# Kernel tuning notes

Measured on AMD Instinct MI355X. Metric: run time of the kernel, lower is better.

The kernel has to match this reference:

```python
import jax, jax.numpy as jnp
import numpy as np

H, B, T, DH = 16, 2, 2048, 64
MODEL_DIM = 1024


def setup_inputs() -> dict:
    key = jax.random.key(0)
    ks = jax.random.split(key, 5)
    q = jax.random.normal(ks[0], (H, B, T, DH), dtype=jnp.float32)
    k = jax.random.normal(ks[1], (H, B, T, DH), dtype=jnp.float32)
    v = jax.random.normal(ks[2], (H, B, T, DH), dtype=jnp.float32)
    Wo_w = jax.random.normal(ks[3], (MODEL_DIM, H * DH), dtype=jnp.float32) * 0.02
    Wo_b = jax.random.normal(ks[4], (MODEL_DIM,), dtype=jnp.float32) * 0.02
    return {"q": q, "k": k, "v": v, "Wo_w": Wo_w, "Wo_b": Wo_b}


def reference(q, k, v, Wo_w, Wo_b):
    # per-head scaled dot-product attention; scale uses per-head dk (=DH)
    scale = jnp.sqrt(jnp.asarray(DH, dtype=q.dtype))
    # scores: [H, B, T, T]
    scores = jnp.einsum('hbtd,hbsd->hbts', q, k) / scale
    # causal mask (additive -1e12 on strict upper triangle, matching torch code)
    mask = jnp.triu(jnp.ones((T, T), dtype=bool), 1)
    scores = scores + (-1e12) * mask.astype(scores.dtype)
    weights = jax.nn.softmax(scores, axis=-1)
    # context per head: [H, B, T, DH]
    context = jnp.einsum('hbts,hbsd->hbtd', weights, v)
    # concat heads along feature dim: [B, T, H*DH]
    context = jnp.transpose(context, (1, 2, 0, 3)).reshape(B, T, H * DH)
    # output projection (torch Linear: x @ W.T + b)
    return context @ Wo_w.T + Wo_b
```

## Files before the change

### kernel.cpp

```cpp
#include <hip/hip_runtime.h>

typedef __attribute__((ext_vector_type(8))) short bf16x8;
typedef __attribute__((ext_vector_type(4))) float f32x4;
typedef __attribute__((ext_vector_type(4))) unsigned int u32x4;
typedef __attribute__((ext_vector_type(2))) unsigned int u32x2;
typedef __attribute__((ext_vector_type(4))) unsigned short u16x4;

#define H_ 16
#define B_ 2
#define T_ 2048
#define DH_ 64
#define MD_ 1024

static __device__ inline unsigned short f2bf(float f) {
    union { float f; unsigned u; } x; x.f = f;
    unsigned r = (x.u + 0x7fffu + ((x.u >> 16) & 1u)) >> 16;
    return (unsigned short)r;
}
static __device__ inline unsigned int pack_bf2(float lo, float hi) {
    return __builtin_amdgcn_perm(__float_as_uint(hi), __float_as_uint(lo), 0x07060302u);
}
static __device__ inline float fexp2(float x) {
#if __has_builtin(__builtin_amdgcn_exp2f)
    return __builtin_amdgcn_exp2f(x);
#else
    return exp2f(x);
#endif
}

__global__ __launch_bounds__(256) void prep_k(const float* __restrict__ k,
                                              const float* __restrict__ v,
                                              const float* __restrict__ w,
                                              unsigned short* __restrict__ kb,
                                              unsigned short* __restrict__ vtb,
                                              unsigned short* __restrict__ wob,
                                              int* __restrict__ fl) {
    __shared__ __attribute__((aligned(16))) unsigned short vt64[64][64];
    const int blk = blockIdx.x;
    const int tid = threadIdx.x;
    if (blk < 1024) {
        int i = (blk * 256 + tid) * 4;
        f32x4 x = *(const f32x4*)(w + i);
        u16x4 y;
        y[0] = f2bf(x[0]); y[1] = f2bf(x[1]); y[2] = f2bf(x[2]); y[3] = f2bf(x[3]);
        *(u16x4*)(wob + i) = y;
    } else if (blk < 2048) {
        int j = blk - 1024;
        const int hb = j >> 5, s0 = (j & 31) * 64;
        const int row = tid >> 2, c = (tid & 3) * 16;
        const long off = (long)hb * (T_ * DH_) + (long)(s0 + row) * DH_ + c;
        const float* p = k + off;
        f32x4 a0 = *(const f32x4*)p;
        f32x4 a1 = *(const f32x4*)(p + 4);
        f32x4 a2 = *(const f32x4*)(p + 8);
        f32x4 a3 = *(const f32x4*)(p + 12);
        u32x4 w0, w1;
        w0[0] = pack_bf2(a0[0], a0[1]); w0[1] = pack_bf2(a0[2], a0[3]);
        w0[2] = pack_bf2(a1[0], a1[1]); w0[3] = pack_bf2(a1[2], a1[3]);
        w1[0] = pack_bf2(a2[0], a2[1]); w1[1] = pack_bf2(a2[2], a2[3]);
        w1[2] = pack_bf2(a3[0], a3[1]); w1[3] = pack_bf2(a3[2], a3[3]);
        *(u32x4*)(kb + off) = w0;
        *(u32x4*)(kb + off + 8) = w1;
    } else if (blk < 3072) {
        int j = blk - 2048;
        const int hb = j >> 5, s0 = (j & 31) * 64;
        const int vkp = tid & 31, vdg = tid >> 5;
        const float* vp = v + (long)hb * (T_ * DH_) + (long)(s0 + 2 * vkp) * DH_ + vdg * 8;
        f32x4 va0 = *(const f32x4*)vp;
        f32x4 va1 = *(const f32x4*)(vp + 4);
        f32x4 vb0 = *(const f32x4*)(vp + DH_);
        f32x4 vb1 = *(const f32x4*)(vp + DH_ + 4);
#pragma unroll
        for (int jj = 0; jj < 4; jj++) {
            ((unsigned int*)&vt64[vdg * 8 + jj][0])[vkp]     = pack_bf2(va0[jj], vb0[jj]);
            ((unsigned int*)&vt64[vdg * 8 + 4 + jj][0])[vkp] = pack_bf2(va1[jj], vb1[jj]);
        }
        __syncthreads();
        const int dh = tid >> 2, kc = (tid & 3) * 16;
        u32x4 o0 = *(const u32x4*)&vt64[dh][kc];
        u32x4 o1 = *(const u32x4*)&vt64[dh][kc + 8];
        unsigned short* op = vtb + (long)hb * (DH_ * T_) + (long)dh * T_ + s0 + kc;
        *(u32x4*)op = o0;
        *(u32x4*)(op + 8) = o1;
    } else {
        for (int z = tid; z < 512; z += 256) fl[z] = 0;
    }
}

#define SE(t, lo, hi) ((unsigned)((t) | ((lo) << 8) | ((hi) << 16)))
__constant__ unsigned sched48[48] = {
    SE(31,0,16), SE(31,16,32), SE(30,15,31), SE(15,0,16),
    SE(30,0,15), SE(29,0,15), SE(29,15,30), SE(28,14,29), SE(14,0,15),
    SE(28,0,14), SE(27,0,14), SE(27,14,28), SE(26,13,27), SE(13,0,14),
    SE(26,0,13), SE(25,0,13), SE(25,13,26), SE(24,12,25), SE(12,0,13),
    SE(24,0,12), SE(23,0,12), SE(23,12,24), SE(22,11,23), SE(11,0,12),
    SE(22,0,11), SE(21,0,11), SE(21,11,22), SE(20,10,21), SE(10,0,11),
    SE(20,0,10), SE(19,0,10), SE(19,10,20), SE(18,9,19), SE(9,0,10),
    SE(18,0,9), SE(17,0,9), SE(17,9,18), SE(16,8,17), SE(8,0,9),
    SE(16,0,8), SE(7,0,8),
    SE(6,0,7), SE(5,0,6), SE(4,0,5), SE(3,0,4), SE(2,0,3), SE(1,0,2), SE(0,0,1)
};

__global__ __launch_bounds__(256, 4) void attn_k(const float* __restrict__ q,
                                                 const unsigned short* __restrict__ kb,
                                                 const unsigned short* __restrict__ vtb,
                                                 unsigned short* __restrict__ ctx,
                                                 float* __restrict__ Op,
                                                 float* __restrict__ lp,
                                                 int* __restrict__ fl) {
    const int i = blockIdx.x;
    const int xcd = i & 7, j = i >> 3;
    const int l = j & 3, idx = j >> 2;
    const unsigned e = sched48[idx];
    const int t  = (int)(e & 255u);
    const int lo = (int)((e >> 8) & 255u);
    const int hi = (int)(e >> 16);
    const int hb = xcd * 4 + l;
    const int h = hb >> 1, b = hb & 1;
    const int tid = threadIdx.x;
    const int wave = tid >> 6, lane = tid & 63;
    const int ln = lane & 15, quad = lane >> 4;

    __shared__ __attribute__((aligned(16))) unsigned short kt[64][72];
    __shared__ __attribute__((aligned(16))) unsigned short vt[64][72];
    __shared__ __attribute__((aligned(16))) unsigned short pl[4][16][72];
    __shared__ int sh_who;

    const long kbase = (long)hb * (T_ * DH_);
    const long vbase = (long)hb * (DH_ * T_);
    const int q0w = t * 64 + wave * 16;
    const int srow = tid >> 2, sc = (tid & 3) * 16;

    bf16x8 qf0, qf1;
    {
        const float qs = 0.18033688011112042f;
        const float* qp = q + kbase + (long)(q0w + ln) * DH_ + quad * 8;
        f32x4 a0 = *(const f32x4*)qp;
        f32x4 a1 = *(const f32x4*)(qp + 4);
        f32x4 b0 = *(const f32x4*)(qp + 32);
        f32x4 b1 = *(const f32x4*)(qp + 36);
#pragma unroll
        for (int z = 0; z < 4; z++) {
            qf0[z]   = (short)f2bf(a0[z] * qs);
            qf0[4+z] = (short)f2bf(a1[z] * qs);
            qf1[z]   = (short)f2bf(b0[z] * qs);
            qf1[4+z] = (short)f2bf(b1[z] * qs);
        }
    }

    f32x4 oT[4];
#pragma unroll
    for (int z = 0; z < 4; z++) oT[z] = f32x4{0.f, 0.f, 0.f, 0.f};
    float lsum = 0.f;

    u32x4 kr0, kr1, vr0, vr1;
    {
        const unsigned short* kp = kb + kbase + (long)(lo * 64 + srow) * DH_ + sc;
        kr0 = *(const u32x4*)kp; kr1 = *(const u32x4*)(kp + 8);
        const unsigned short* vp = vtb + vbase + (long)srow * T_ + lo * 64 + sc;
        vr0 = *(const u32x4*)vp; vr1 = *(const u32x4*)(vp + 8);
    }

#pragma unroll 1
    for (int step = lo; step < hi; step++) {
        __syncthreads();
        *(u32x4*)&kt[srow][sc]     = kr0;
        *(u32x4*)&kt[srow][sc + 8] = kr1;
        *(u32x4*)&vt[srow][sc]     = vr0;
        *(u32x4*)&vt[srow][sc + 8] = vr1;
        __syncthreads();

        if (step + 1 < hi) {
            const unsigned short* kp = kb + kbase + (long)((step + 1) * 64 + srow) * DH_ + sc;
            kr0 = *(const u32x4*)kp; kr1 = *(const u32x4*)(kp + 8);
            const unsigned short* vp = vtb + vbase + (long)srow * T_ + (step + 1) * 64 + sc;
            vr0 = *(const u32x4*)vp; vr1 = *(const u32x4*)(vp + 8);
        }

        f32x4 sa[4];
#pragma unroll
        for (int nt = 0; nt < 4; nt++) {
            bf16x8 kf0 = *(const bf16x8*)&kt[nt * 16 + ln][quad * 8];
            bf16x8 kf1 = *(const bf16x8*)&kt[nt * 16 + ln][32 + quad * 8];
            f32x4 a = f32x4{0.f, 0.f, 0.f, 0.f};
            a = __builtin_amdgcn_mfma_f32_16x16x32_bf16(kf0, qf0, a, 0, 0, 0);
            a = __builtin_amdgcn_mfma_f32_16x16x32_bf16(kf1, qf1, a, 0, 0, 0);
            sa[nt] = a;
        }

        if (step == t) {
            const int qi = wave * 16 + ln;
#pragma unroll
            for (int nt = 0; nt < 4; nt++)
#pragma unroll
                for (int r = 0; r < 4; r++) {
                    float p = fexp2(sa[nt][r]);
                    if (nt * 16 + quad * 4 + r > qi) p = 0.f;
                    sa[nt][r] = p;
                }
        } else {
#pragma unroll
            for (int nt = 0; nt < 4; nt++)
#pragma unroll
                for (int r = 0; r < 4; r++)
                    sa[nt][r] = fexp2(sa[nt][r]);
        }

#pragma unroll
        for (int nt = 0; nt < 4; nt++)
            lsum += (sa[nt][0] + sa[nt][1]) + (sa[nt][2] + sa[nt][3]);

#pragma unroll
        for (int nt = 0; nt < 4; nt++) {
            u32x2 ww;
            ww[0] = pack_bf2(sa[nt][0], sa[nt][1]);
            ww[1] = pack_bf2(sa[nt][2], sa[nt][3]);
            *(u32x2*)&pl[wave][ln][nt * 16 + quad * 4] = ww;
        }

        bf16x8 pf0 = *(const bf16x8*)&pl[wave][ln][quad * 8];
        bf16x8 pf1 = *(const bf16x8*)&pl[wave][ln][32 + quad * 8];

#pragma unroll
        for (int dt = 0; dt < 4; dt++) {
            bf16x8 vf0 = *(const bf16x8*)&vt[dt * 16 + ln][quad * 8];
            bf16x8 vf1 = *(const bf16x8*)&vt[dt * 16 + ln][32 + quad * 8];
            oT[dt] = __builtin_amdgcn_mfma_f32_16x16x32_bf16(vf0, pf0, oT[dt], 0, 0, 0);
            oT[dt] = __builtin_amdgcn_mfma_f32_16x16x32_bf16(vf1, pf1, oT[dt], 0, 0, 0);
        }
    }

    lsum += __shfl_xor(lsum, 16);
    lsum += __shfl_xor(lsum, 32);

    float rl;
    if (t < 16) {
        rl = __builtin_amdgcn_rcpf(lsum);
    } else {
        const int c = (lo != 0) ? 1 : 0;
        const long slab = (((long)c * 32 + hb) * 16 + (t - 16));
        float* ob = Op + slab * 4096;
        const int qlocal = wave * 16 + ln;
#pragma unroll
        for (int dt = 0; dt < 4; dt++)
#pragma unroll
            for (int r = 0; r < 4; r++)
                __hip_atomic_store(&ob[(dt * 16 + quad * 4 + r) * 64 + qlocal], oT[dt][r],
                                   __ATOMIC_RELAXED, __HIP_MEMORY_SCOPE_AGENT);
        if (quad == 0)
            __hip_atomic_store(&lp[slab * 64 + qlocal], lsum,
                               __ATOMIC_RELAXED, __HIP_MEMORY_SCOPE_AGENT);
        __syncthreads();
        if (tid == 0)
            sh_who = __hip_atomic_fetch_add(&fl[hb * 16 + (t - 16)], 1,
                                            __ATOMIC_RELAXED, __HIP_MEMORY_SCOPE_AGENT);
        __syncthreads();
        if (sh_who != 1) return;
        const long slab2 = (((long)(c ^ 1) * 32 + hb) * 16 + (t - 16));
        const float* qb = Op + slab2 * 4096;
#pragma unroll
        for (int dt = 0; dt < 4; dt++)
#pragma unroll
            for (int r = 0; r < 4; r++)
                oT[dt][r] += __hip_atomic_load(&qb[(dt * 16 + quad * 4 + r) * 64 + qlocal],
                                               __ATOMIC_RELAXED, __HIP_MEMORY_SCOPE_AGENT);
        lsum += __hip_atomic_load(&lp[slab2 * 64 + qlocal],
                                  __ATOMIC_RELAXED, __HIP_MEMORY_SCOPE_AGENT);
        rl = __builtin_amdgcn_rcpf(lsum);
    }

#pragma unroll
    for (int dt = 0; dt < 4; dt++) {
        u16x4 y;
        y[0] = f2bf(oT[dt][0] * rl); y[1] = f2bf(oT[dt][1] * rl);
        y[2] = f2bf(oT[dt][2] * rl); y[3] = f2bf(oT[dt][3] * rl);
        *(u16x4*)&pl[wave][ln][dt * 16 + quad * 4] = y;
    }
    const int rr = lane >> 2, cc = (lane & 3) * 16;
    u32x4 z0 = *(const u32x4*)&pl[wave][rr][cc];
    u32x4 z1 = *(const u32x4*)&pl[wave][rr][cc + 8];
    unsigned short* cp = ctx + (long)(b * T_ + t * 64 + wave * 16 + rr) * MD_ + h * 64 + cc;
    *(u32x4*)cp = z0;
    *(u32x4*)(cp + 8) = z1;
}

__global__ __launch_bounds__(256, 4) void proj_k(const unsigned short* __restrict__ A,
                                                 const unsigned short* __restrict__ Bw,
                                                 const float* __restrict__ bias,
                                                 float* __restrict__ out) {
    const int i = blockIdx.x;
    const int n0 = ((i & 7) * 2 + ((i >> 3) & 1)) * 64;
    const int m0 = (i >> 4) * 64;
    const int tid = threadIdx.x;
    const int wave = tid >> 6, lane = tid & 63;
    const int ln = lane & 15, quad = lane >> 4;

    __shared__ __attribute__((aligned(16))) unsigned short As[64][72];
    __shared__ __attribute__((aligned(16))) unsigned short Bs[64][72];

    const int srow = tid >> 2, sc = (tid & 3) * 16;

    f32x4 acc[4];
#pragma unroll
    for (int z = 0; z < 4; z++) acc[z] = f32x4{0.f, 0.f, 0.f, 0.f};

    u32x4 ar0, ar1, br0, br1;
    {
        const unsigned short* ap = A + (long)(m0 + srow) * 1024 + sc;
        ar0 = *(const u32x4*)ap; ar1 = *(const u32x4*)(ap + 8);
        const unsigned short* bp = Bw + (long)(n0 + srow) * 1024 + sc;
        br0 = *(const u32x4*)bp; br1 = *(const u32x4*)(bp + 8);
    }

#pragma unroll 1
    for (int ks = 0; ks < 1024; ks += 64) {
        __syncthreads();
        *(u32x4*)&As[srow][sc]     = ar0;
        *(u32x4*)&As[srow][sc + 8] = ar1;
        *(u32x4*)&Bs[srow][sc]     = br0;
        *(u32x4*)&Bs[srow][sc + 8] = br1;
        __syncthreads();

        if (ks + 64 < 1024) {
            const unsigned short* ap = A + (long)(m0 + srow) * 1024 + ks + 64 + sc;
            ar0 = *(const u32x4*)ap; ar1 = *(const u32x4*)(ap + 8);
            const unsigned short* bp = Bw + (long)(n0 + srow) * 1024 + ks + 64 + sc;
            br0 = *(const u32x4*)bp; br1 = *(const u32x4*)(bp + 8);
        }

        bf16x8 bf0 = *(const bf16x8*)&Bs[wave * 16 + ln][quad * 8];
        bf16x8 bf1 = *(const bf16x8*)&Bs[wave * 16 + ln][32 + quad * 8];
#pragma unroll
        for (int mt = 0; mt < 4; mt++) {
            bf16x8 af0 = *(const bf16x8*)&As[mt * 16 + ln][quad * 8];
            bf16x8 af1 = *(const bf16x8*)&As[mt * 16 + ln][32 + quad * 8];
            acc[mt] = __builtin_amdgcn_mfma_f32_16x16x32_bf16(af0, bf0, acc[mt], 0, 0, 0);
            acc[mt] = __builtin_amdgcn_mfma_f32_16x16x32_bf16(af1, bf1, acc[mt], 0, 0, 0);
        }
    }

    int col = n0 + wave * 16 + ln;
    float bz = bias[col];
#pragma unroll
    for (int mt = 0; mt < 4; mt++)
#pragma unroll
        for (int r = 0; r < 4; r++) {
            int row = m0 + mt * 16 + quad * 4 + r;
            out[(long)row * 1024 + col] = acc[mt][r] + bz;
        }
}

extern "C" void kernel_launch(void* const* d_in, const int* in_sizes, int n_in,
                              void* d_out, int out_size, void* d_ws, size_t ws_size,
                              hipStream_t stream) {
    const float* q    = (const float*)d_in[0];
    const float* k    = (const float*)d_in[1];
    const float* v    = (const float*)d_in[2];
    const float* Wo_w = (const float*)d_in[3];
    const float* Wo_b = (const float*)d_in[4];
    float* out = (float*)d_out;

    unsigned short* ctx = (unsigned short*)d_ws;
    unsigned short* wob = ctx + (size_t)4096 * 1024;
    unsigned short* kbb = wob + (size_t)1024 * 1024;
    unsigned short* vtb = kbb + (size_t)32 * 2048 * 64;
    float* Opart = (float*)(vtb + (size_t)32 * 2048 * 64);
    float* lpart = Opart + (size_t)2 * 32 * 16 * 64 * 64;
    int*   flags = (int*)(lpart + (size_t)2 * 32 * 16 * 64);

    prep_k<<<3073, 256, 0, stream>>>(k, v, Wo_w, kbb, vtb, wob, flags);
    attn_k<<<1536, 256, 0, stream>>>(q, kbb, vtb, ctx, Opart, lpart, flags);
    proj_k<<<1024, 256, 0, stream>>>(ctx, wob, Wo_b, out);
}
```

Measured before the change: 150.8 us.

## Double attention query tile to 128 rows and rebalance causal work schedule

Each attention block now processes 128 query rows, with each wave handling two 16-row subtiles, so every K/V tile staged in shared memory feeds twice as many MFMAs. The static causal schedule is rebuilt as a 3-slot by 8-type table so work balances across CUs with 768 blocks, and long rows are still split in two with a combine through partial buffers. Occupancy drops to 3 blocks per CU, register pressure rises from the doubled accumulators, and fully masked K tiles are skipped per wave.

```diff
diff --git a/kernel.cpp b/kernel.cpp
--- a/kernel.cpp
+++ b/kernel.cpp
@@ -83,25 +83,21 @@
         *(u32x4*)op = o0;
         *(u32x4*)(op + 8) = o1;
     } else {
-        for (int z = tid; z < 512; z += 256) fl[z] = 0;
-    }
-}
-
-#define SE(t, lo, hi) ((unsigned)((t) | ((lo) << 8) | ((hi) << 16)))
-__constant__ unsigned sched48[48] = {
-    SE(31,0,16), SE(31,16,32), SE(30,15,31), SE(15,0,16),
-    SE(30,0,15), SE(29,0,15), SE(29,15,30), SE(28,14,29), SE(14,0,15),
-    SE(28,0,14), SE(27,0,14), SE(27,14,28), SE(26,13,27), SE(13,0,14),
-    SE(26,0,13), SE(25,0,13), SE(25,13,26), SE(24,12,25), SE(12,0,13),
-    SE(24,0,12), SE(23,0,12), SE(23,12,24), SE(22,11,23), SE(11,0,12),
-    SE(22,0,11), SE(21,0,11), SE(21,11,22), SE(20,10,21), SE(10,0,11),
-    SE(20,0,10), SE(19,0,10), SE(19,10,20), SE(18,9,19), SE(9,0,10),
-    SE(18,0,9), SE(17,0,9), SE(17,9,18), SE(16,8,17), SE(8,0,9),
-    SE(16,0,8), SE(7,0,8),
-    SE(6,0,7), SE(5,0,6), SE(4,0,5), SE(3,0,4), SE(2,0,3), SE(1,0,2), SE(0,0,1)
+        for (int z = tid; z < 256; z += 256) fl[z] = 0;
+    }
+}
+
+#define SE2(t, lo, hi) ((unsigned)((t) | ((lo) << 4) | ((hi) << 10)))
+__constant__ unsigned sched24[3][8] = {
+    { SE2(15,0,16), SE2(7,0,16), SE2(14,0,15), SE2(14,15,30),
+      SE2(13,0,14), SE2(13,14,28), SE2(12,13,26), SE2(11,12,24) },
+    { SE2(15,16,32), SE2(6,0,14), SE2(12,0,13), SE2(10,0,11),
+      SE2(10,11,22), SE2(9,0,10), SE2(11,0,12), SE2(5,0,12) },
+    { SE2(0,0,2), SE2(1,0,4), SE2(2,0,6), SE2(3,0,8),
+      SE2(8,0,9), SE2(9,10,20), SE2(8,9,18), SE2(4,0,10) },
 };
 
-__global__ __launch_bounds__(256, 4) void attn_k(const float* __restrict__ q,
+__global__ __launch_bounds__(256, 3) void attn_k(const float* __restrict__ q,
                                                  const unsigned short* __restrict__ kb,
                                                  const unsigned short* __restrict__ vtb,
                                                  unsigned short* __restrict__ ctx,
@@ -110,12 +106,13 @@
                                                  int* __restrict__ fl) {
     const int i = blockIdx.x;
     const int xcd = i & 7, j = i >> 3;
-    const int l = j & 3, idx = j >> 2;
-    const unsigned e = sched48[idx];
-    const int t  = (int)(e & 255u);
-    const int lo = (int)((e >> 8) & 255u);
-    const int hi = (int)(e >> 16);
-    const int hb = xcd * 4 + l;
+    const int cu = j & 31, slot = j >> 5;
+    const int type = cu >> 2, hbl = cu & 3;
+    const unsigned e = sched24[slot][type];
+    const int t  = (int)(e & 15u);
+    const int lo = (int)((e >> 4) & 63u);
+    const int hi = (int)(e >> 10);
+    const int hb = xcd * 4 + hbl;
     const int h = hb >> 1, b = hb & 1;
     const int tid = threadIdx.x;
     const int wave = tid >> 6, lane = tid & 63;
@@ -123,35 +120,44 @@
 
     __shared__ __attribute__((aligned(16))) unsigned short kt[64][72];
     __shared__ __attribute__((aligned(16))) unsigned short vt[64][72];
-    __shared__ __attribute__((aligned(16))) unsigned short pl[4][16][72];
+    __shared__ __attribute__((aligned(16))) unsigned short pl[4][32][72];
     __shared__ int sh_who;
 
     const long kbase = (long)hb * (T_ * DH_);
     const long vbase = (long)hb * (DH_ * T_);
-    const int q0w = t * 64 + wave * 16;
+    const int q0w = t * 128 + wave * 32;
     const int srow = tid >> 2, sc = (tid & 3) * 16;
 
-    bf16x8 qf0, qf1;
+    bf16x8 qf00, qf01, qf10, qf11;
     {
         const float qs = 0.18033688011112042f;
-        const float* qp = q + kbase + (long)(q0w + ln) * DH_ + quad * 8;
-        f32x4 a0 = *(const f32x4*)qp;
-        f32x4 a1 = *(const f32x4*)(qp + 4);
-        f32x4 b0 = *(const f32x4*)(qp + 32);
-        f32x4 b1 = *(const f32x4*)(qp + 36);
+        const float* qp0 = q + kbase + (long)(q0w + ln) * DH_ + quad * 8;
+        const float* qp1 = qp0 + 16 * DH_;
+        f32x4 a0 = *(const f32x4*)qp0;
+        f32x4 a1 = *(const f32x4*)(qp0 + 4);
+        f32x4 b0 = *(const f32x4*)(qp0 + 32);
+        f32x4 b1 = *(const f32x4*)(qp0 + 36);
+        f32x4 c0 = *(const f32x4*)qp1;
+        f32x4 c1 = *(const f32x4*)(qp1 + 4);
+        f32x4 d0 = *(const f32x4*)(qp1 + 32);
+        f32x4 d1 = *(const f32x4*)(qp1 + 36);
 #pragma unroll
         for (int z = 0; z < 4; z++) {
-            qf0[z]   = (short)f2bf(a0[z] * qs);
-            qf0[4+z] = (short)f2bf(a1[z] * qs);
-            qf1[z]   = (short)f2bf(b0[z] * qs);
-            qf1[4+z] = (short)f2bf(b1[z] * qs);
-        }
-    }
-
-    f32x4 oT[4];
-#pragma unroll
-    for (int z = 0; z < 4; z++) oT[z] = f32x4{0.f, 0.f, 0.f, 0.f};
-    float lsum = 0.f;
+            qf00[z]   = (short)f2bf(a0[z] * qs);
+            qf00[4+z] = (short)f2bf(a1[z] * qs);
+            qf01[z]   = (short)f2bf(b0[z] * qs);
+            qf01[4+z] = (short)f2bf(b1[z] * qs);
+            qf10[z]   = (short)f2bf(c0[z] * qs);
+            qf10[4+z] = (short)f2bf(c1[z] * qs);
+            qf11[z]   = (short)f2bf(d0[z] * qs);
+            qf11[4+z] = (short)f2bf(d1[z] * qs);
+        }
+    }
+
+    f32x4 oT0[4], oT1[4];
+#pragma unroll
+    for (int z = 0; z < 4; z++) { oT0[z] = f32x4{0.f,0.f,0.f,0.f}; oT1[z] = f32x4{0.f,0.f,0.f,0.f}; }
+    float lsum0 = 0.f, lsum1 = 0.f;
 
     u32x4 kr0, kr1, vr0, vr1;
     {
@@ -177,111 +183,129 @@
             vr0 = *(const u32x4*)vp; vr1 = *(const u32x4*)(vp + 8);
         }
 
-        f32x4 sa[4];
-#pragma unroll
-        for (int nt = 0; nt < 4; nt++) {
-            bf16x8 kf0 = *(const bf16x8*)&kt[nt * 16 + ln][quad * 8];
-            bf16x8 kf1 = *(const bf16x8*)&kt[nt * 16 + ln][32 + quad * 8];
-            f32x4 a = f32x4{0.f, 0.f, 0.f, 0.f};
-            a = __builtin_amdgcn_mfma_f32_16x16x32_bf16(kf0, qf0, a, 0, 0, 0);
-            a = __builtin_amdgcn_mfma_f32_16x16x32_bf16(kf1, qf1, a, 0, 0, 0);
-            sa[nt] = a;
-        }
-
-        if (step == t) {
-            const int qi = wave * 16 + ln;
-#pragma unroll
-            for (int nt = 0; nt < 4; nt++)
-#pragma unroll
-                for (int r = 0; r < 4; r++) {
-                    float p = fexp2(sa[nt][r]);
-                    if (nt * 16 + quad * 4 + r > qi) p = 0.f;
-                    sa[nt][r] = p;
+        if (step * 64 <= q0w + 31) {
+            const bool dmask = (step * 64 + 63 > q0w);
+            const int dbase = step * 64 + quad * 4 - q0w - ln;
+
+#pragma unroll
+            for (int nt = 0; nt < 4; nt++) {
+                bf16x8 kf0 = *(const bf16x8*)&kt[nt * 16 + ln][quad * 8];
+                bf16x8 kf1 = *(const bf16x8*)&kt[nt * 16 + ln][32 + quad * 8];
+                f32x4 a0 = f32x4{0.f,0.f,0.f,0.f};
+                a0 = __builtin_amdgcn_mfma_f32_16x16x32_bf16(kf0, qf00, a0, 0, 0, 0);
+                a0 = __builtin_amdgcn_mfma_f32_16x16x32_bf16(kf1, qf01, a0, 0, 0, 0);
+                f32x4 a1 = f32x4{0.f,0.f,0.f,0.f};
+                a1 = __builtin_amdgcn_mfma_f32_16x16x32_bf16(kf0, qf10, a1, 0, 0, 0);
+                a1 = __builtin_amdgcn_mfma_f32_16x16x32_bf16(kf1, qf11, a1, 0, 0, 0);
+#pragma unroll
+                for (int r = 0; r < 4; r++) { a0[r] = fexp2(a0[r]); a1[r] = fexp2(a1[r]); }
+                if (dmask) {
+#pragma unroll
+                    for (int r = 0; r < 4; r++) {
+                        if (dbase + nt * 16 + r > 0)  a0[r] = 0.f;
+                        if (dbase + nt * 16 + r > 16) a1[r] = 0.f;
+                    }
                 }
-        } else {
-#pragma unroll
-            for (int nt = 0; nt < 4; nt++)
-#pragma unroll
-                for (int r = 0; r < 4; r++)
-                    sa[nt][r] = fexp2(sa[nt][r]);
-        }
-
-#pragma unroll
-        for (int nt = 0; nt < 4; nt++)
-            lsum += (sa[nt][0] + sa[nt][1]) + (sa[nt][2] + sa[nt][3]);
-
-#pragma unroll
-        for (int nt = 0; nt < 4; nt++) {
-            u32x2 ww;
-            ww[0] = pack_bf2(sa[nt][0], sa[nt][1]);
-            ww[1] = pack_bf2(sa[nt][2], sa[nt][3]);
-            *(u32x2*)&pl[wave][ln][nt * 16 + quad * 4] = ww;
-        }
-
-        bf16x8 pf0 = *(const bf16x8*)&pl[wave][ln][quad * 8];
-        bf16x8 pf1 = *(const bf16x8*)&pl[wave][ln][32 + quad * 8];
-
-#pragma unroll
-        for (int dt = 0; dt < 4; dt++) {
-            bf16x8 vf0 = *(const bf16x8*)&vt[dt * 16 + ln][quad * 8];
-            bf16x8 vf1 = *(const bf16x8*)&vt[dt * 16 + ln][32 + quad * 8];
-            oT[dt] = __builtin_amdgcn_mfma_f32_16x16x32_bf16(vf0, pf0, oT[dt], 0, 0, 0);
-            oT[dt] = __builtin_amdgcn_mfma_f32_16x16x32_bf16(vf1, pf1, oT[dt], 0, 0, 0);
-        }
-    }
-
-    lsum += __shfl_xor(lsum, 16);
-    lsum += __shfl_xor(lsum, 32);
-
-    float rl;
-    if (t < 16) {
-        rl = __builtin_amdgcn_rcpf(lsum);
+                lsum0 += (a0[0] + a0[1]) + (a0[2] + a0[3]);
+                lsum1 += (a1[0] + a1[1]) + (a1[2] + a1[3]);
+                u32x2 w0, w1;
+                w0[0] = pack_bf2(a0[0], a0[1]); w0[1] = pack_bf2(a0[2], a0[3]);
+                w1[0] = pack_bf2(a1[0], a1[1]); w1[1] = pack_bf2(a1[2], a1[3]);
+                *(u32x2*)&pl[wave][ln][nt * 16 + quad * 4]      = w0;
+                *(u32x2*)&pl[wave][16 + ln][nt * 16 + quad * 4] = w1;
+            }
+
+            bf16x8 pf00 = *(const bf16x8*)&pl[wave][ln][quad * 8];
+            bf16x8 pf01 = *(const bf16x8*)&pl[wave][ln][32 + quad * 8];
+            bf16x8 pf10 = *(const bf16x8*)&pl[wave][16 + ln][quad * 8];
+            bf16x8 pf11 = *(const bf16x8*)&pl[wave][16 + ln][32 + quad * 8];
+
+#pragma unroll
+            for (int dt = 0; dt < 4; dt++) {
+                bf16x8 vf0 = *(const bf16x8*)&vt[dt * 16 + ln][quad * 8];
+                bf16x8 vf1 = *(const bf16x8*)&vt[dt * 16 + ln][32 + quad * 8];
+                oT0[dt] = __builtin_amdgcn_mfma_f32_16x16x32_bf16(vf0, pf00, oT0[dt], 0, 0, 0);
+                oT0[dt] = __builtin_amdgcn_mfma_f32_16x16x32_bf16(vf1, pf01, oT0[dt], 0, 0, 0);
+                oT1[dt] = __builtin_amdgcn_mfma_f32_16x16x32_bf16(vf0, pf10, oT1[dt], 0, 0, 0);
+                oT1[dt] = __builtin_amdgcn_mfma_f32_16x16x32_bf16(vf1, pf11, oT1[dt], 0, 0, 0);
+            }
+        }
+    }
+
+    lsum0 += __shfl_xor(lsum0, 16); lsum0 += __shfl_xor(lsum0, 32);
+    lsum1 += __shfl_xor(lsum1, 16); lsum1 += __shfl_xor(lsum1, 32);
+
+    float rl0, rl1;
+    if (t < 8) {
+        rl0 = __builtin_amdgcn_rcpf(lsum0);
+        rl1 = __builtin_amdgcn_rcpf(lsum1);
     } else {
         const int c = (lo != 0) ? 1 : 0;
-        const long slab = (((long)c * 32 + hb) * 16 + (t - 16));
-        float* ob = Op + slab * 4096;
-        const int qlocal = wave * 16 + ln;
+        const long slab = ((long)c * 32 + hb) * 8 + (t - 8);
+        float* ob = Op + slab * 8192;
+        const int ql0 = wave * 32 + ln, ql1 = ql0 + 16;
 #pragma unroll
         for (int dt = 0; dt < 4; dt++)
 #pragma unroll
-            for (int r = 0; r < 4; r++)
-                __hip_atomic_store(&ob[(dt * 16 + quad * 4 + r) * 64 + qlocal], oT[dt][r],
+            for (int r = 0; r < 4; r++) {
+                const int dh = dt * 16 + quad * 4 + r;
+                __hip_atomic_store(&ob[dh * 128 + ql0], oT0[dt][r],
                                    __ATOMIC_RELAXED, __HIP_MEMORY_SCOPE_AGENT);
-        if (quad == 0)
-            __hip_atomic_store(&lp[slab * 64 + qlocal], lsum,
+                __hip_atomic_store(&ob[dh * 128 + ql1], oT1[dt][r],
+                                   __ATOMIC_RELAXED, __HIP_MEMORY_SCOPE_AGENT);
+            }
+        if (quad == 0) {
+            __hip_atomic_store(&lp[slab * 128 + ql0], lsum0,
                                __ATOMIC_RELAXED, __HIP_MEMORY_SCOPE_AGENT);
+            __hip_atomic_store(&lp[slab * 128 + ql1], lsum1,
+                               __ATOMIC_RELAXED, __HIP_MEMORY_SCOPE_AGENT);
+        }
         __syncthreads();
         if (tid == 0)
-            sh_who = __hip_atomic_fetch_add(&fl[hb * 16 + (t - 16)], 1,
+            sh_who = __hip_atomic_fetch_add(&fl[hb * 8 + (t - 8)], 1,
                                             __ATOMIC_RELAXED, __HIP_MEMORY_SCOPE_AGENT);
         __syncthreads();
         if (sh_who != 1) return;
-        const long slab2 = (((long)(c ^ 1) * 32 + hb) * 16 + (t - 16));
-        const float* qb = Op + slab2 * 4096;
+        const long slab2 = ((long)(c ^ 1) * 32 + hb) * 8 + (t - 8);
+        const float* qb = Op + slab2 * 8192;
 #pragma unroll
         for (int dt = 0; dt < 4; dt++)
 #pragma unroll
-            for (int r = 0; r < 4; r++)
-                oT[dt][r] += __hip_atomic_load(&qb[(dt * 16 + quad * 4 + r) * 64 + qlocal],
-                                               __ATOMIC_RELAXED, __HIP_MEMORY_SCOPE_AGENT);
-        lsum += __hip_atomic_load(&lp[slab2 * 64 + qlocal],
-                                  __ATOMIC_RELAXED, __HIP_MEMORY_SCOPE_AGENT);
-        rl = __builtin_amdgcn_rcpf(lsum);
+            for (int r = 0; r < 4; r++) {
+                const int dh = dt * 16 + quad * 4 + r;
+                oT0[dt][r] += __hip_atomic_load(&qb[dh * 128 + ql0],
+                                                __ATOMIC_RELAXED, __HIP_MEMORY_SCOPE_AGENT);
+                oT1[dt][r] += __hip_atomic_load(&qb[dh * 128 + ql1],
+                                                __ATOMIC_RELAXED, __HIP_MEMORY_SCOPE_AGENT);
+            }
+        lsum0 += __hip_atomic_load(&lp[slab2 * 128 + ql0],
+                                   __ATOMIC_RELAXED, __HIP_MEMORY_SCOPE_AGENT);
+        lsum1 += __hip_atomic_load(&lp[slab2 * 128 + ql1],
+                                   __ATOMIC_RELAXED, __HIP_MEMORY_SCOPE_AGENT);
+        rl0 = __builtin_amdgcn_rcpf(lsum0);
+        rl1 = __builtin_amdgcn_rcpf(lsum1);
     }
 
 #pragma unroll
     for (int dt = 0; dt < 4; dt++) {
-        u16x4 y;
-        y[0] = f2bf(oT[dt][0] * rl); y[1] = f2bf(oT[dt][1] * rl);
-        y[2] = f2bf(oT[dt][2] * rl); y[3] = f2bf(oT[dt][3] * rl);
-        *(u16x4*)&pl[wave][ln][dt * 16 + quad * 4] = y;
-    }
-    const int rr = lane >> 2, cc = (lane & 3) * 16;
+        u16x4 y0, y1;
+        y0[0] = f2bf(oT0[dt][0] * rl0); y0[1] = f2bf(oT0[dt][1] * rl0);
+        y0[2] = f2bf(oT0[dt][2] * rl0); y0[3] = f2bf(oT0[dt][3] * rl0);
+        y1[0] = f2bf(oT1[dt][0] * rl1); y1[1] = f2bf(oT1[dt][1] * rl1);
+        y1[2] = f2bf(oT1[dt][2] * rl1); y1[3] = f2bf(oT1[dt][3] * rl1);
+        *(u16x4*)&pl[wave][ln][dt * 16 + quad * 4]      = y0;
+        *(u16x4*)&pl[wave][16 + ln][dt * 16 + quad * 4] = y1;
+    }
+    const int rr = lane >> 1, cc = (lane & 1) * 32;
     u32x4 z0 = *(const u32x4*)&pl[wave][rr][cc];
     u32x4 z1 = *(const u32x4*)&pl[wave][rr][cc + 8];
-    unsigned short* cp = ctx + (long)(b * T_ + t * 64 + wave * 16 + rr) * MD_ + h * 64 + cc;
+    u32x4 z2 = *(const u32x4*)&pl[wave][rr][cc + 16];
+    u32x4 z3 = *(const u32x4*)&pl[wave][rr][cc + 24];
+    unsigned short* cp = ctx + (long)(b * T_ + t * 128 + wave * 32 + rr) * MD_ + h * 64 + cc;
     *(u32x4*)cp = z0;
     *(u32x4*)(cp + 8) = z1;
+    *(u32x4*)(cp + 16) = z2;
+    *(u32x4*)(cp + 24) = z3;
 }
 
 __global__ __launch_bounds__(256, 4) void proj_k(const unsigned short* __restrict__ A,
@@ -365,10 +389,10 @@
     unsigned short* kbb = wob + (size_t)1024 * 1024;
     unsigned short* vtb = kbb + (size_t)32 * 2048 * 64;
     float* Opart = (float*)(vtb + (size_t)32 * 2048 * 64);
-    float* lpart = Opart + (size_t)2 * 32 * 16 * 64 * 64;
-    int*   flags = (int*)(lpart + (size_t)2 * 32 * 16 * 64);
+    float* lpart = Opart + (size_t)2 * 32 * 8 * 64 * 128;
+    int*   flags = (int*)(lpart + (size_t)2 * 32 * 8 * 128);
 
     prep_k<<<3073, 256, 0, stream>>>(k, v, Wo_w, kbb, vtb, wob, flags);
-    attn_k<<<1536, 256, 0, stream>>>(q, kbb, vtb, ctx, Opart, lpart, flags);
+    attn_k<<<768, 256, 0, stream>>>(q, kbb, vtb, ctx, Opart, lpart, flags);
     proj_k<<<1024, 256, 0, stream>>>(ctx, wob, Wo_b, out);
 }
```

Result: no change. 150.5 us (-0.2%).
